# Optimization experiments

Hardware: AMD Instinct MI355X
Metric: run time of the kernel (lower is better)

Reference implementation:

```python
import jax, jax.numpy as jnp
import numpy as np

TAU = 10.0
N, D = 4096, 8192  # batch, feature dim (D >= N required by the original indexing)
NUM_CLASSES = 100


def setup_inputs() -> dict:
    key = jax.random.key(0)
    k1, k2 = jax.random.split(key)
    embeddings = jax.random.normal(k1, (N, D), dtype=jnp.float32)
    labels = jax.random.randint(k2, (N,), 0, NUM_CLASSES, dtype=jnp.int64)
    return {"embeddings": embeddings, "labels": labels}


def reference(embeddings, labels):
    # Faithful to the original (buggy) torch math:
    # inner_product[i, d] = exp(emb[i, d]**2 / tau)  (trailing singleton dim dropped)
    n = embeddings.shape[0]
    A = jnp.exp(embeddings * embeddings / TAU)          # [N, D]
    # denominator_i = sum_d A[i, d] - A[i, i]
    denom = jnp.sum(A, axis=1) - jnp.diagonal(A)[:n]    # [N]
    # numerator terms: exp(A[i, j] / tau) for j in batch indices (j < N <= D)
    B = jnp.exp(A[:, :n] / TAU)                          # [N, N]
    same = labels[:, None] == labels[None, :]            # [N, N]
    mask = same & ~jnp.eye(n, dtype=bool)
    counts = jnp.sum(mask, axis=1).astype(embeddings.dtype)   # misma_clase per i
    suma = jnp.sum(jnp.where(mask, B, jnp.zeros((), B.dtype)), axis=1) / denom  # [N]
    return jnp.sum(jnp.log(suma / counts))
```

## Files before the change

### kernel.cpp

```cpp
#include <hip/hip_runtime.h>

static constexpr int N = 4096;
static constexpr int D = 8192;
static constexpr int BLOCK = 256;

__global__ __launch_bounds__(BLOCK) void supcon_rows(
    const float* __restrict__ emb,
    const int* __restrict__ labels,
    float* __restrict__ row_out)
{
    const int row = blockIdx.x;
    const int tid = threadIdx.x;
    const int lab_i = labels[row];
    const float4* rowp = reinterpret_cast<const float4*>(emb + (size_t)row * D);
    const int4* labp = reinterpret_cast<const int4*>(labels);

    float4 v[8];
    #pragma unroll
    for (int it = 0; it < 8; ++it)
        v[it] = rowp[tid + it * BLOCK];
    int4 lj[4];
    #pragma unroll
    for (int it = 0; it < 4; ++it)
        lj[it] = labp[tid + it * BLOCK];

    float denom = 0.f, ssum = 0.f, diag = 0.f, fcnt = 0.f;

    #pragma unroll
    for (int it = 0; it < 4; ++it) {
        const int j0 = (tid + it * BLOCK) * 4;
        float xs[4] = {v[it].x, v[it].y, v[it].z, v[it].w};
        int   ls[4] = {lj[it].x, lj[it].y, lj[it].z, lj[it].w};
        #pragma unroll
        for (int k = 0; k < 4; ++k) {
            float a = __expf(xs[k] * xs[k] * 0.1f);
            denom += a;
            float b = __expf(a * 0.1f);
            bool match = (ls[k] == lab_i) && (j0 + k != row);
            ssum += match ? b : 0.f;
            fcnt += match ? 1.f : 0.f;
            diag += (j0 + k == row) ? a : 0.f;
        }
    }
    #pragma unroll
    for (int it = 4; it < 8; ++it) {
        float xs[4] = {v[it].x, v[it].y, v[it].z, v[it].w};
        #pragma unroll
        for (int k = 0; k < 4; ++k)
            denom += __expf(xs[k] * xs[k] * 0.1f);
    }

    #pragma unroll
    for (int off = 32; off > 0; off >>= 1) {
        denom += __shfl_down(denom, off);
        ssum  += __shfl_down(ssum,  off);
        diag  += __shfl_down(diag,  off);
        fcnt  += __shfl_down(fcnt,  off);
    }

    __shared__ float s_red[4][4];
    const int wave = tid >> 6;
    if ((tid & 63) == 0) {
        s_red[0][wave] = denom;
        s_red[1][wave] = ssum;
        s_red[2][wave] = diag;
        s_red[3][wave] = fcnt;
    }
    __syncthreads();
    if (tid == 0) {
        float dn = 0.f, sv = 0.f, dg = 0.f, c = 0.f;
        #pragma unroll
        for (int w = 0; w < 4; ++w) {
            dn += s_red[0][w]; sv += s_red[1][w]; dg += s_red[2][w]; c += s_red[3][w];
        }
        dn -= dg;
        row_out[row] = __logf(sv) - __logf(dn) - __logf(c);
    }
}

__global__ __launch_bounds__(1024) void reduce_rows(
    const float* __restrict__ row_vals, float* __restrict__ out)
{
    const int tid = threadIdx.x;
    float4 x = reinterpret_cast<const float4*>(row_vals)[tid];
    float s = x.x + x.y + x.z + x.w;
    #pragma unroll
    for (int off = 32; off > 0; off >>= 1)
        s += __shfl_down(s, off);
    __shared__ float sb[16];
    if ((tid & 63) == 0) sb[tid >> 6] = s;
    __syncthreads();
    if (tid == 0) {
        float t = 0.f;
        #pragma unroll
        for (int w = 0; w < 16; ++w) t += sb[w];
        *out = t;
    }
}

extern "C" void kernel_launch(void* const* d_in, const int* in_sizes, int n_in,
                              void* d_out, int out_size, void* d_ws, size_t ws_size,
                              hipStream_t stream) {
    const float* emb  = (const float*)d_in[0];
    const int* labels = (const int*)d_in[1];
    float* out        = (float*)d_out;
    float* row_vals   = (float*)d_ws;

    supcon_rows<<<dim3(N), dim3(BLOCK), 0, stream>>>(emb, labels, row_vals);
    reduce_rows<<<dim3(1), dim3(1024), 0, stream>>>(row_vals, out);
}
```

Before: 187.5 us.

## Process four rows per block with double-buffered register prefetch

Each block now handles four rows instead of one. While one row is being computed, the next row is loaded into a second register buffer, and the label vector is loaded once per block instead of once per row. The goal is to hide global memory latency and cut redundant label reads and block launch overhead. In exchange it doubles register pressure (launch bounds request 4 blocks per CU) and shrinks the grid to 1024 blocks, which could reduce occupancy or load balance across the 256 CUs.

```diff
diff --git a/kernel.cpp b/kernel.cpp
--- a/kernel.cpp
+++ b/kernel.cpp
@@ -3,27 +3,22 @@
 static constexpr int N = 4096;
 static constexpr int D = 8192;
 static constexpr int BLOCK = 256;
+static constexpr int RPB = 4;
+static constexpr int GRID = N / RPB;
 
-__global__ __launch_bounds__(BLOCK) void supcon_rows(
-    const float* __restrict__ emb,
-    const int* __restrict__ labels,
-    float* __restrict__ row_out)
+__device__ __forceinline__ void load_row(float4 (&v)[8], const float* __restrict__ emb,
+                                         int row, int tid)
 {
-    const int row = blockIdx.x;
-    const int tid = threadIdx.x;
-    const int lab_i = labels[row];
     const float4* rowp = reinterpret_cast<const float4*>(emb + (size_t)row * D);
-    const int4* labp = reinterpret_cast<const int4*>(labels);
-
-    float4 v[8];
     #pragma unroll
     for (int it = 0; it < 8; ++it)
         v[it] = rowp[tid + it * BLOCK];
-    int4 lj[4];
-    #pragma unroll
-    for (int it = 0; it < 4; ++it)
-        lj[it] = labp[tid + it * BLOCK];
+}
 
+__device__ __forceinline__ void compute_row(const float4 (&v)[8], const int4 (&lj)[4],
+                                            int lab_i, int row, int tid, int r,
+                                            float (*s_red)[4][4])
+{
     float denom = 0.f, ssum = 0.f, diag = 0.f, fcnt = 0.f;
 
     #pragma unroll
@@ -57,24 +52,58 @@
         diag  += __shfl_down(diag,  off);
         fcnt  += __shfl_down(fcnt,  off);
     }
-
-    __shared__ float s_red[4][4];
     const int wave = tid >> 6;
     if ((tid & 63) == 0) {
-        s_red[0][wave] = denom;
-        s_red[1][wave] = ssum;
-        s_red[2][wave] = diag;
-        s_red[3][wave] = fcnt;
+        s_red[r][0][wave] = denom;
+        s_red[r][1][wave] = ssum;
+        s_red[r][2][wave] = diag;
+        s_red[r][3][wave] = fcnt;
     }
+}
+
+__global__ __launch_bounds__(BLOCK, 4) void supcon_rows(
+    const float* __restrict__ emb,
+    const int* __restrict__ labels,
+    float* __restrict__ row_out)
+{
+    __shared__ float s_red[RPB][4][4];
+    const int tid  = threadIdx.x;
+    const int row0 = blockIdx.x * RPB;
+
+    const int4* labp = reinterpret_cast<const int4*>(labels);
+    int4 lj[4];
+    #pragma unroll
+    for (int it = 0; it < 4; ++it)
+        lj[it] = labp[tid + it * BLOCK];
+
+    int labr[RPB];
+    #pragma unroll
+    for (int r = 0; r < RPB; ++r)
+        labr[r] = labels[row0 + r];
+
+    float4 va[8], vb[8];
+    load_row(va, emb, row0 + 0, tid);
+    load_row(vb, emb, row0 + 1, tid);
+
+    compute_row(va, lj, labr[0], row0 + 0, tid, 0, s_red);
+    load_row(va, emb, row0 + 2, tid);
+    compute_row(vb, lj, labr[1], row0 + 1, tid, 1, s_red);
+    load_row(vb, emb, row0 + 3, tid);
+    compute_row(va, lj, labr[2], row0 + 2, tid, 2, s_red);
+    compute_row(vb, lj, labr[3], row0 + 3, tid, 3, s_red);
+
     __syncthreads();
-    if (tid == 0) {
+    if (tid < RPB) {
         float dn = 0.f, sv = 0.f, dg = 0.f, c = 0.f;
         #pragma unroll
         for (int w = 0; w < 4; ++w) {
-            dn += s_red[0][w]; sv += s_red[1][w]; dg += s_red[2][w]; c += s_red[3][w];
+            dn += s_red[tid][0][w];
+            sv += s_red[tid][1][w];
+            dg += s_red[tid][2][w];
+            c  += s_red[tid][3][w];
         }
         dn -= dg;
-        row_out[row] = __logf(sv) - __logf(dn) - __logf(c);
+        row_out[row0 + tid] = __logf(sv) - __logf(dn) - __logf(c);
     }
 }
 
@@ -106,6 +135,6 @@
     float* out        = (float*)d_out;
     float* row_vals   = (float*)d_ws;
 
-    supcon_rows<<<dim3(N), dim3(BLOCK), 0, stream>>>(emb, labels, row_vals);
+    supcon_rows<<<dim3(GRID), dim3(BLOCK), 0, stream>>>(emb, labels, row_vals);
     reduce_rows<<<dim3(1), dim3(1024), 0, stream>>>(row_vals, out);
 }
```

Measured after the change: 193.0 us. 1.03x slower.
